# Kernel tuning notes

Hardware: AMD Instinct MI355X
Metric: run time of the kernel (lower is better)

## Reference

```python
import jax, jax.numpy as jnp
import numpy as np

EMBED = 1024
HEADS = 16
HEAD_DIM = EMBED // HEADS


def setup_inputs() -> dict:
    key = jax.random.key(0)
    ks = jax.random.split(key, 9)
    N, S = 2, 2048
    values = jax.random.normal(ks[0], (N, S, EMBED), dtype=jnp.float32)
    keys = jax.random.normal(ks[1], (N, S, EMBED), dtype=jnp.float32)
    queries = jax.random.normal(ks[2], (N, S, EMBED), dtype=jnp.float32)
    mask = jax.random.randint(ks[3], (N, 1, S, S), 0, 2, dtype=jnp.int32)
    sc_h = 1.0 / np.sqrt(HEAD_DIM)
    sc_e = 1.0 / np.sqrt(EMBED)
    Wv = jax.random.normal(ks[4], (HEAD_DIM, HEAD_DIM), dtype=jnp.float32) * sc_h
    Wk = jax.random.normal(ks[5], (HEAD_DIM, HEAD_DIM), dtype=jnp.float32) * sc_h
    Wq = jax.random.normal(ks[6], (HEAD_DIM, HEAD_DIM), dtype=jnp.float32) * sc_h
    Wo = jax.random.normal(ks[7], (EMBED, EMBED), dtype=jnp.float32) * sc_e
    bo = jax.random.normal(ks[8], (EMBED,), dtype=jnp.float32) * 0.01
    return {"values": values, "keys": keys, "queries": queries, "mask": mask,
            "Wv": Wv, "Wk": Wk, "Wq": Wq, "Wo": Wo, "bo": bo}


def reference(values, keys, queries, mask, Wv, Wk, Wq, Wo, bo):
    N, S, _ = queries.shape
    H, D = HEADS, HEAD_DIM
    # split heads: [N, S, H, D]
    v = values.reshape(N, -1, H, D) @ Wv.T
    k = keys.reshape(N, -1, H, D) @ Wk.T
    q = queries.reshape(N, -1, H, D) @ Wq.T
    # [N, H, Q, K] scores
    energy = jnp.einsum('nqhd,nkhd->nhqk', q, k)
    energy = jnp.where(mask == 0, jnp.float32(1e-12), energy)
    attention = jax.nn.softmax(energy / np.sqrt(D), axis=3)
    # faithful to source einsum 'NVHD,NHQK->NQHD' (sums V and K independently)
    out = jnp.einsum('nvhd,nhqk->nqhd', v, attention).reshape(N, S, H * D)
    return out @ Wo.T + bo
```

## Files before the change

kernel.cpp:

```cpp
#include <hip/hip_runtime.h>

#define NB     2
#define SEQ    2048
#define EMBED  1024
#define HEADS  16
#define HDIM   64
#define CH     256
#define ROWS   (SEQ / CH)

__global__ __launch_bounds__(256) void colsum_part(const float* __restrict__ vals,
                                                   float* __restrict__ part) {
    const int b = blockIdx.x;
    const int n = b / CH;
    const int c = b % CH;
    const int t = threadIdx.x;
    const float4* base = reinterpret_cast<const float4*>(vals)
                       + (size_t)(n * SEQ + c * ROWS) * (EMBED / 4);
    float4 acc = make_float4(0.f, 0.f, 0.f, 0.f);
    #pragma unroll
    for (int r = 0; r < ROWS; ++r) {
        float4 v = base[(size_t)r * (EMBED / 4) + t];
        acc.x += v.x; acc.y += v.y; acc.z += v.z; acc.w += v.w;
    }
    reinterpret_cast<float4*>(part)[(size_t)(n * CH + c) * (EMBED / 4) + t] = acc;
}

__global__ __launch_bounds__(256) void matvec_k(const float* __restrict__ part,
                                                const float* __restrict__ Wv,
                                                const float* __restrict__ Wo,
                                                const float* __restrict__ bo,
                                                float* __restrict__ row) {
    const int n    = blockIdx.x >> 5;
    const int oblk = blockIdx.x & 31;
    __shared__ float svl[EMBED];
    __shared__ float vfl[EMBED];
    const int t = threadIdx.x;

    {
        const float4* p = reinterpret_cast<const float4*>(part)
                        + (size_t)n * CH * (EMBED / 4) + t;
        float4 acc = make_float4(0.f, 0.f, 0.f, 0.f);
        #pragma unroll 8
        for (int c = 0; c < CH; ++c) {
            float4 v = p[(size_t)c * (EMBED / 4)];
            acc.x += v.x; acc.y += v.y; acc.z += v.z; acc.w += v.w;
        }
        reinterpret_cast<float4*>(svl)[t] = acc;
    }
    __syncthreads();

    for (int o = t; o < EMBED; o += 256) {
        const int h = o >> 6, d = o & 63;
        const float* wr = Wv + d * HDIM;
        const float* sr = svl + h * HDIM;
        float a = 0.f;
        #pragma unroll
        for (int e = 0; e < HDIM; ++e) a += wr[e] * sr[e];
        vfl[o] = a;
    }
    __syncthreads();

    const int wave = t >> 6;
    const int lane = t & 63;
    float4 vv[4];
    #pragma unroll
    for (int it = 0; it < 4; ++it)
        vv[it] = reinterpret_cast<const float4*>(vfl)[it * 64 + lane];

    const float4* Wo4 = reinterpret_cast<const float4*>(Wo);
    #pragma unroll
    for (int j = 0; j < 8; ++j) {
        const int o = oblk * 32 + wave * 8 + j;
        float acc = 0.f;
        #pragma unroll
        for (int it = 0; it < 4; ++it) {
            float4 w4 = Wo4[(size_t)o * (EMBED / 4) + it * 64 + lane];
            acc += w4.x * vv[it].x + w4.y * vv[it].y
                 + w4.z * vv[it].z + w4.w * vv[it].w;
        }
        #pragma unroll
        for (int off = 32; off >= 1; off >>= 1)
            acc += __shfl_xor(acc, off);
        if (lane == 0) row[n * EMBED + o] = acc + bo[o];
    }
}

__global__ __launch_bounds__(256) void bcast_k(const float* __restrict__ row,
                                               float4* __restrict__ out4) {
    const int b  = blockIdx.x;
    const int n  = b >> 7;
    const int r0 = (b & 127) * 16;
    const float4 v =
        reinterpret_cast<const float4*>(row)[n * (EMBED / 4) + threadIdx.x];
    float4* o = out4 + (size_t)(n * SEQ + r0) * (EMBED / 4) + threadIdx.x;
    #pragma unroll
    for (int r = 0; r < 16; ++r)
        o[(size_t)r * (EMBED / 4)] = v;
}

extern "C" void kernel_launch(void* const* d_in, const int* in_sizes, int n_in,
                              void* d_out, int out_size, void* d_ws, size_t ws_size,
                              hipStream_t stream) {
    const float* vals = (const float*)d_in[0];
    const float* Wv   = (const float*)d_in[4];
    const float* Wo   = (const float*)d_in[7];
    const float* bo   = (const float*)d_in[8];
    float* out = (float*)d_out;

    float* part = (float*)d_ws;
    float* row  = part + (size_t)NB * CH * EMBED;

    colsum_part<<<NB * CH, 256, 0, stream>>>(vals, part);
    matvec_k<<<NB * (EMBED / 32), 256, 0, stream>>>(part, Wv, Wo, bo, row);
    bcast_k<<<256, 256, 0, stream>>>(row, (float4*)out);
}
```

Measured before the change: 147.1 us.

## Fuse matvec and broadcast kernels, halve colsum partial chunks

Merges the Wo matvec and the output broadcast into one kernel, so each block computes 16 output columns and writes them across all 2048 rows. This removes one launch and the round-trip of the row vector through global memory. The colsum pass now uses 128 chunks instead of 256, which gives fewer blocks but less partial data to reduce. In exchange, each fused block recomputes the full column-sum reduction and the Wv product, and every broadcast store covers only 64 bytes per row, so writes are less contiguous.

```diff
diff --git a/kernel.cpp b/kernel.cpp
--- a/kernel.cpp
+++ b/kernel.cpp
@@ -5,40 +5,42 @@
 #define EMBED  1024
 #define HEADS  16
 #define HDIM   64
-#define CH     256
+#define CH     128
 #define ROWS   (SEQ / CH)
 
 __global__ __launch_bounds__(256) void colsum_part(const float* __restrict__ vals,
                                                    float* __restrict__ part) {
     const int b = blockIdx.x;
-    const int n = b / CH;
-    const int c = b % CH;
+    const int n = b >> 7;
+    const int c = b & 127;
     const int t = threadIdx.x;
     const float4* base = reinterpret_cast<const float4*>(vals)
                        + (size_t)(n * SEQ + c * ROWS) * (EMBED / 4);
     float4 acc = make_float4(0.f, 0.f, 0.f, 0.f);
-    #pragma unroll
+    #pragma unroll 8
     for (int r = 0; r < ROWS; ++r) {
         float4 v = base[(size_t)r * (EMBED / 4) + t];
         acc.x += v.x; acc.y += v.y; acc.z += v.z; acc.w += v.w;
     }
-    reinterpret_cast<float4*>(part)[(size_t)(n * CH + c) * (EMBED / 4) + t] = acc;
+    reinterpret_cast<float4*>(part)[(size_t)b * (EMBED / 4) + t] = acc;
 }
 
-__global__ __launch_bounds__(256) void matvec_k(const float* __restrict__ part,
+__global__ __launch_bounds__(256) void mv_bcast(const float* __restrict__ part,
                                                 const float* __restrict__ Wv,
                                                 const float* __restrict__ Wo,
                                                 const float* __restrict__ bo,
-                                                float* __restrict__ row) {
-    const int n    = blockIdx.x >> 5;
-    const int oblk = blockIdx.x & 31;
+                                                float4* __restrict__ out4) {
+    const int b   = blockIdx.x;
+    const int wn  = b >> 6;
+    const int s16 = b & 63;
+    const int t   = threadIdx.x;
     __shared__ float svl[EMBED];
     __shared__ float vfl[EMBED];
-    const int t = threadIdx.x;
+    __shared__ float rsl[16];
 
     {
         const float4* p = reinterpret_cast<const float4*>(part)
-                        + (size_t)n * CH * (EMBED / 4) + t;
+                        + (size_t)wn * CH * (EMBED / 4) + t;
         float4 acc = make_float4(0.f, 0.f, 0.f, 0.f);
         #pragma unroll 8
         for (int c = 0; c < CH; ++c) {
@@ -69,8 +71,8 @@
 
     const float4* Wo4 = reinterpret_cast<const float4*>(Wo);
     #pragma unroll
-    for (int j = 0; j < 8; ++j) {
-        const int o = oblk * 32 + wave * 8 + j;
+    for (int j = 0; j < 4; ++j) {
+        const int o = s16 * 16 + wave * 4 + j;
         float acc = 0.f;
         #pragma unroll
         for (int it = 0; it < 4; ++it) {
@@ -81,21 +83,16 @@
         #pragma unroll
         for (int off = 32; off >= 1; off >>= 1)
             acc += __shfl_xor(acc, off);
-        if (lane == 0) row[n * EMBED + o] = acc + bo[o];
+        if (lane == 0) rsl[wave * 4 + j] = acc + bo[o];
     }
-}
+    __syncthreads();
 
-__global__ __launch_bounds__(256) void bcast_k(const float* __restrict__ row,
-                                               float4* __restrict__ out4) {
-    const int b  = blockIdx.x;
-    const int n  = b >> 7;
-    const int r0 = (b & 127) * 16;
-    const float4 v =
-        reinterpret_cast<const float4*>(row)[n * (EMBED / 4) + threadIdx.x];
-    float4* o = out4 + (size_t)(n * SEQ + r0) * (EMBED / 4) + threadIdx.x;
-    #pragma unroll
-    for (int r = 0; r < 16; ++r)
-        o[(size_t)r * (EMBED / 4)] = v;
+    const float4 val = reinterpret_cast<const float4*>(rsl)[t & 3];
+    float4* o = out4 + (size_t)wn * SEQ * (EMBED / 4) + (s16 * 4 + (t & 3))
+              + (size_t)(t >> 2) * (EMBED / 4);
+    #pragma unroll 8
+    for (int k = 0; k < 32; ++k)
+        o[(size_t)k * 64 * (EMBED / 4)] = val;
 }
 
 extern "C" void kernel_launch(void* const* d_in, const int* in_sizes, int n_in,
@@ -108,9 +105,7 @@
     float* out = (float*)d_out;
 
     float* part = (float*)d_ws;
-    float* row  = part + (size_t)NB * CH * EMBED;
 
     colsum_part<<<NB * CH, 256, 0, stream>>>(vals, part);
-    matvec_k<<<NB * (EMBED / 32), 256, 0, stream>>>(part, Wv, Wo, bo, row);
-    bcast_k<<<256, 256, 0, stream>>>(row, (float4*)out);
+    mv_bcast<<<NB * 64, 256, 0, stream>>>(part, Wv, Wo, bo, (float4*)out);
 }
```

New measurement: 136.4 us. 7.3% less time.
